# Kernel optimization log

Measured on AMD Instinct MI355X. Metric: run time of the kernel, lower is better.

## Reference

```python
import jax, jax.numpy as jnp
import numpy as np

TOPK = 8
NGRAM = 3
D = 256
VOCAB = 5000


def build_scores_mask(seq_len, topk, ngram):
    # Replicates PREFIX.__init__ mask construction then the [:S*k,:S*k] slice
    # and the ~(...) inversion: True = disallowed (masked out).
    # Chunk-level: query chunk i may attend key chunks j in [i-1, i+ngram-2], j != i.
    L = seq_len
    allowed = np.zeros((L, L), dtype=bool)
    for i in range(L):
        for j in range(max(0, i - 1), min(L, i + ngram - 1)):
            if j != i:
                allowed[i, j] = True
    tok = np.kron(allowed, np.ones((topk, topk), dtype=bool))  # (L*k, L*k)
    return jnp.asarray(~tok)


def setup_inputs() -> dict:
    key = jax.random.key(0)
    k1, k2, k3, k4 = jax.random.split(key, 4)
    bsz, seq_len = 64, 128
    na_pred = jax.random.normal(k1, (bsz, seq_len, VOCAB), dtype=jnp.float32)
    emb_table = jax.random.normal(k2, (VOCAB, D), dtype=jnp.float32) * 0.02
    Wq = jax.random.normal(k3, (D, D), dtype=jnp.float32) / np.sqrt(D)
    Wk = jax.random.normal(k4, (D, D), dtype=jnp.float32) / np.sqrt(D)
    bq = jnp.zeros((D,), dtype=jnp.float32)
    bk = jnp.zeros((D,), dtype=jnp.float32)
    return {"bsz": bsz, "seq_len": seq_len, "na_pred": na_pred,
            "emb_table": emb_table, "Wq": Wq, "bq": bq, "Wk": Wk, "bk": bk}


def reference(bsz, seq_len, na_pred, emb_table, Wq, bq, Wk, bk):
    k, g = TOPK, NGRAM
    # top-k prefix candidates and their renormalized probabilities
    probs = jax.nn.softmax(na_pred, axis=-1)                 # (b, S, V)
    na_prefix_prob, na_prefix = jax.lax.top_k(probs, k)     # (b, S, k)
    na_prefix_prob = jax.nn.softmax(na_prefix_prob, axis=-1)
    # gather prefix embeddings (espnet-style sqrt(d) scale)
    prefix_emb = emb_table[na_prefix] * jnp.asarray(np.sqrt(D), na_pred.dtype)  # (b,S,k,D)
    prefix_emb = prefix_emb.reshape(bsz, seq_len * k, D)
    # ScoreAttention over gathered prefixes with ngram block mask
    q = prefix_emb @ Wq + bq
    kk = prefix_emb @ Wk + bk
    scores = jnp.einsum('bqd,bkd->bqk', q, kk) / jnp.asarray(np.sqrt(D), q.dtype)
    mask = build_scores_mask(seq_len, k, g)                  # (S*k, S*k) True=masked
    scores = jnp.where(mask[None], jnp.asarray(-1e9, scores.dtype), scores)
    attn = jax.nn.softmax(scores, axis=-1)                   # (b, S*k, S*k)
    # per-candidate score = incoming attention mass
    na_score = attn.sum(axis=1).reshape(bsz, seq_len, k)
    # elementwise mul with candidate prob, L1 normalize (F.normalize p=1 eps=1e-12)
    prefix_score = na_score * na_prefix_prob
    l1 = jnp.maximum(jnp.sum(jnp.abs(prefix_score), axis=-1, keepdims=True), 1e-12)
    prefix_score = prefix_score / l1                         # (b, S, k)
    # weighted reduce over candidates
    prefix_emb4 = prefix_emb.reshape(bsz, seq_len, k, D)
    scored_prefix = jnp.sum(prefix_emb4 * prefix_score[..., None], axis=2)  # (b, S, D)
    return scored_prefix, prefix_score, na_prefix
```

## Files before the change

### kernel.cpp

```cpp
#include <hip/hip_runtime.h>
#include <math.h>

#define TOPK 8
#define D    256
#define VOCAB 5000
#define BSZ  64
#define SEQ  128
#define ROWS (BSZ*SEQ)
#define NF4  (VOCAB/4)

#define OFF_IDX   0
#define OFF_NPP   262144
#define OFF_M     524288
#define OFF_W     787456
#define OFF_P     790528
#define OFF_NPART 5910528
#define OFF_KBV   6434816

#define OUT_SCORED 0
#define OUT_PS     2097152
#define OUT_IDX    2162688

typedef unsigned long long u64;
typedef unsigned int u32;

__device__ __forceinline__ float wave_fmax(float v) {
    #pragma unroll
    for (int st = 1; st < 64; st <<= 1) v = fmaxf(v, __shfl_xor(v, st, 64));
    return v;
}
__device__ __forceinline__ float wave_fsum(float v) {
    #pragma unroll
    for (int st = 1; st < 64; st <<= 1) v += __shfl_xor(v, st, 64);
    return v;
}
__device__ __forceinline__ u64 wave_umax(u64 v) {
    #pragma unroll
    for (int st = 1; st < 64; st <<= 1) {
        const u64 o = __shfl_xor(v, st, 64);
        v = (o > v) ? o : v;
    }
    return v;
}
__device__ __forceinline__ u64 pack_key(float x, int idx) {
    u32 bu = __float_as_uint(x);
    u32 key = bu ^ ((u32)((int)bu >> 31) | 0x80000000u);
    return ((u64)key << 32) | (u64)(0xFFFFFFFFu ^ (u32)idx);
}

__global__ __launch_bounds__(256) void topk_kernel(
    const float* __restrict__ na_pred,
    int*  __restrict__ out_idx,
    float* __restrict__ out_npp,
    float* __restrict__ out_idx_f)
{
    __shared__ float tmax[256];
    __shared__ float wsum[4];
    __shared__ float cv[64];
    __shared__ int   ci[64];
    __shared__ int   cnt;
    __shared__ u64   res_s[8];
    __shared__ u64   ured[4];

    const int tid  = threadIdx.x;
    const int lane = tid & 63;
    const int wid  = tid >> 6;
    const long long base = (long long)blockIdx.x * VOCAB;
    const float4* src = (const float4*)(na_pred + base);

    if (tid == 0) cnt = 0;

    const int i0 = tid, i1 = tid + 256, i2 = tid + 512, i3 = tid + 768, i4 = tid + 1024;
    const float4 r0 = src[i0];
    const float4 r1 = src[i1];
    const float4 r2 = src[i2];
    const float4 r3 = src[i3];
    const float4 r4 = (i4 < NF4) ? src[i4]
                    : make_float4(-INFINITY, -INFINITY, -INFINITY, -INFINITY);

    float m01 = fmaxf(fmaxf(r0.x, r0.y), fmaxf(r0.z, r0.w));
    float m23 = fmaxf(fmaxf(r1.x, r1.y), fmaxf(r1.z, r1.w));
    float m45 = fmaxf(fmaxf(r2.x, r2.y), fmaxf(r2.z, r2.w));
    float m67 = fmaxf(fmaxf(r3.x, r3.y), fmaxf(r3.z, r3.w));
    float m89 = fmaxf(fmaxf(r4.x, r4.y), fmaxf(r4.z, r4.w));
    const float m = fmaxf(fmaxf(fmaxf(m01, m23), fmaxf(m45, m67)), m89);
    tmax[tid] = m;
    __syncthreads();

    const float comb = fmaxf(fmaxf(tmax[lane], tmax[lane + 64]),
                             fmaxf(tmax[lane + 128], tmax[lane + 192]));
    const float rowmax = wave_fmax(comb);
    float am = comb, thr = rowmax;
    #pragma unroll
    for (int r = 0; r < 8; ++r) {
        const float cur = wave_fmax(am);
        if (am == cur) am = -INFINITY;
        thr = cur;
    }

    float se = 0.f;
    se += __expf(r0.x - rowmax); se += __expf(r0.y - rowmax);
    se += __expf(r0.z - rowmax); se += __expf(r0.w - rowmax);
    se += __expf(r1.x - rowmax); se += __expf(r1.y - rowmax);
    se += __expf(r1.z - rowmax); se += __expf(r1.w - rowmax);
    se += __expf(r2.x - rowmax); se += __expf(r2.y - rowmax);
    se += __expf(r2.z - rowmax); se += __expf(r2.w - rowmax);
    se += __expf(r3.x - rowmax); se += __expf(r3.y - rowmax);
    se += __expf(r3.z - rowmax); se += __expf(r3.w - rowmax);
    se += __expf(r4.x - rowmax); se += __expf(r4.y - rowmax);
    se += __expf(r4.z - rowmax); se += __expf(r4.w - rowmax);
    const float swv = wave_fsum(se);
    if (lane == 0) wsum[wid] = swv;

#define FILT(val, eidx) do { const float x_ = (val); \
    if (x_ >= thr) { const int pos = atomicAdd(&cnt, 1); \
        if (pos < 64) { cv[pos] = x_; ci[pos] = (eidx); } } } while (0)
    FILT(r0.x, 4*i0+0); FILT(r0.y, 4*i0+1); FILT(r0.z, 4*i0+2); FILT(r0.w, 4*i0+3);
    FILT(r1.x, 4*i1+0); FILT(r1.y, 4*i1+1); FILT(r1.z, 4*i1+2); FILT(r1.w, 4*i1+3);
    FILT(r2.x, 4*i2+0); FILT(r2.y, 4*i2+1); FILT(r2.z, 4*i2+2); FILT(r2.w, 4*i2+3);
    FILT(r3.x, 4*i3+0); FILT(r3.y, 4*i3+1); FILT(r3.z, 4*i3+2); FILT(r3.w, 4*i3+3);
    FILT(r4.x, 4*i4+0); FILT(r4.y, 4*i4+1); FILT(r4.z, 4*i4+2); FILT(r4.w, 4*i4+3);
#undef FILT
    __syncthreads();

    const int cntv = cnt;
    if (cntv <= 64) {
        if (tid < 64) {
            u64 key = (tid < cntv) ? pack_key(cv[tid], ci[tid]) : 0ULL;
            #pragma unroll
            for (int r = 0; r < 8; ++r) {
                const u64 mm = wave_umax(key);
                if (key == mm) key = 0ULL;
                if (tid == 0) res_s[r] = mm;
            }
        }
    } else {
        u64 last = ~0ULL;
        for (int r = 0; r < 8; ++r) {
            u64 best = 0ULL;
#define CAND(val, eidx) do { const u64 k_ = pack_key((val), (eidx)); \
    if (k_ < last && k_ > best) best = k_; } while (0)
            CAND(r0.x, 4*i0+0); CAND(r0.y, 4*i0+1); CAND(r0.z, 4*i0+2); CAND(r0.w, 4*i0+3);
            CAND(r1.x, 4*i1+0); CAND(r1.y, 4*i1+1); CAND(r1.z, 4*i1+2); CAND(r1.w, 4*i1+3);
            CAND(r2.x, 4*i2+0); CAND(r2.y, 4*i2+1); CAND(r2.z, 4*i2+2); CAND(r2.w, 4*i2+3);
            CAND(r3.x, 4*i3+0); CAND(r3.y, 4*i3+1); CAND(r3.z, 4*i3+2); CAND(r3.w, 4*i3+3);
            CAND(r4.x, 4*i4+0); CAND(r4.y, 4*i4+1); CAND(r4.z, 4*i4+2); CAND(r4.w, 4*i4+3);
#undef CAND
            best = wave_umax(best);
            if (lane == 0) ured[wid] = best;
            __syncthreads();
            u64 b = ured[0];
            #pragma unroll
            for (int wq = 1; wq < 4; ++wq) b = (ured[wq] > b) ? ured[wq] : b;
            if (tid == 0) res_s[r] = b;
            last = b;
            __syncthreads();
        }
    }
    __syncthreads();

    if (wid == 0 && lane < 8) {
        const float S = wsum[0] + wsum[1] + wsum[2] + wsum[3];
        const u64 res = res_s[lane];
        const u32 key = (u32)(res >> 32);
        const int ixv = (int)(0xFFFFFFFFu ^ (u32)(res & 0xFFFFFFFFu));
        const u32 bu  = key ^ ((key & 0x80000000u) ? 0x80000000u : 0xFFFFFFFFu);
        const float p = __expf(__uint_as_float(bu) - rowmax) / S;
        float pm = p;
        #pragma unroll
        for (int st = 1; st < 8; st <<= 1) pm = fmaxf(pm, __shfl_xor(pm, st, 64));
        const float q = __expf(p - pm);
        float s2 = q;
        #pragma unroll
        for (int st = 1; st < 8; st <<= 1) s2 += __shfl_xor(s2, st, 64);
        const long long ob = (long long)blockIdx.x * TOPK + lane;
        out_idx[ob]   = ixv;
        out_npp[ob]   = q / s2;
        out_idx_f[ob] = (float)ixv;
    }
}

__global__ __launch_bounds__(256) void m_kernel(
    const float* __restrict__ Wq, const float* __restrict__ Wk,
    float* __restrict__ M)
{
    __shared__ float qrow[D];
    const int a = blockIdx.x, j = threadIdx.x;
    qrow[j] = Wq[a*D + j];
    __syncthreads();
    float acc = 0.f;
    #pragma unroll 4
    for (int d4 = 0; d4 < 64; ++d4) {
        const float4 wk = *(const float4*)&Wk[j*D + 4*d4];
        const float4 q4 = *(const float4*)&qrow[4*d4];
        acc += wk.x*q4.x + wk.y*q4.y + wk.z*q4.z + wk.w*q4.w;
    }
    M[a*D + j] = acc;
}

__global__ __launch_bounds__(256) void bias_kernel(
    const float* __restrict__ Wk, const float* __restrict__ bq,
    float* __restrict__ w)
{
    const int i = threadIdx.x;
    float aw = 0.f;
    #pragma unroll 4
    for (int d4 = 0; d4 < 64; ++d4) {
        const float4 wk = *(const float4*)&Wk[i*D + 4*d4];
        const float4 b4 = *(const float4*)&bq[4*d4];
        aw += wk.x*b4.x + wk.y*b4.y + wk.z*b4.z + wk.w*b4.w;
    }
    w[i] = aw;
}

__global__ __launch_bounds__(256) void kbv_kernel(
    const float* __restrict__ E, const float* __restrict__ w,
    float* __restrict__ kbv)
{
    const int row  = blockIdx.x * 4 + (threadIdx.x >> 6);
    const int lane = threadIdx.x & 63;
    if (row >= VOCAB) return;
    const float4 e  = *(const float4*)&E[(long long)row*D + 4*lane];
    const float4 ww = *(const float4*)&w[4*lane];
    float p = e.x*ww.x + e.y*ww.y + e.z*ww.z + e.w*ww.w;
    #pragma unroll
    for (int st = 1; st < 64; st <<= 1) p += __shfl_xor(p, st, 64);
    if (lane == 0) kbv[row] = p;
}

__global__ __launch_bounds__(256) void p_kernel(
    const float* __restrict__ E, const float* __restrict__ M,
    float* __restrict__ P)
{
    __shared__ float seT[256][20];
    const int tid = threadIdx.x;
    const int r0  = blockIdx.x * 16;
    {
        const int r = tid >> 4, d4b = tid & 15;
        const bool ok = (r0 + r) < VOCAB;
        #pragma unroll
        for (int k = 0; k < 4; ++k) {
            const int d4 = d4b + 16*k;
            float4 v = make_float4(0.f, 0.f, 0.f, 0.f);
            if (ok) v = *(const float4*)&E[(long long)(r0+r)*D + 4*d4];
            seT[4*d4+0][r] = v.x; seT[4*d4+1][r] = v.y;
            seT[4*d4+2][r] = v.z; seT[4*d4+3][r] = v.w;
        }
    }
    __syncthreads();
    const int rg = tid >> 6, j4 = tid & 63;
    float acc[4][4];
    #pragma unroll
    for (int i = 0; i < 4; ++i)
        { acc[i][0]=0.f; acc[i][1]=0.f; acc[i][2]=0.f; acc[i][3]=0.f; }
    #pragma unroll 4
    for (int d = 0; d < 256; ++d) {
        const float4 m4 = *(const float4*)&M[d*D + 4*j4];
        const float4 s4 = *(const float4*)&seT[d][4*rg];
        const float ss[4] = {s4.x, s4.y, s4.z, s4.w};
        #pragma unroll
        for (int rr = 0; rr < 4; ++rr) {
            acc[rr][0] += ss[rr]*m4.x; acc[rr][1] += ss[rr]*m4.y;
            acc[rr][2] += ss[rr]*m4.z; acc[rr][3] += ss[rr]*m4.w;
        }
    }
    #pragma unroll
    for (int rr = 0; rr < 4; ++rr) {
        const int row = r0 + 4*rg + rr;
        if (row < VOCAB) {
            float4 o;
            o.x = acc[rr][0]; o.y = acc[rr][1]; o.z = acc[rr][2]; o.w = acc[rr][3];
            *(float4*)&P[(long long)row*D + 4*j4] = o;
        }
    }
}

__global__ __launch_bounds__(64) void attn_kernel(
    const float* __restrict__ P, const float* __restrict__ E,
    const int*  __restrict__ idx, const float* __restrict__ kbv,
    float* __restrict__ na_part )
{
    const int blk = blockIdx.x;
    const int b = blk >> 7, s = blk & 127;
    const int tid = threadIdx.x;

    __shared__ float Ps[8][260];
    __shared__ float Es[16][260];
    __shared__ int   qidx[8];
    __shared__ int   kidx[16];
    __shared__ float kb[16];
    __shared__ int   kchs[2];

    int kcl[2]; int nk = 0;
    if (s > 0)       kcl[nk++] = s - 1;
    if (s < SEQ - 1) kcl[nk++] = s + 1;
    const int nkeys = nk * 8;

    if (tid < 2 && tid < nk) kchs[tid] = kcl[tid];
    if (tid < 8) qidx[tid] = idx[blk*8 + tid];
    if (tid < 16) {
        if (tid < nkeys) {
            const int v = idx[(b*SEQ + kcl[tid >> 3])*8 + (tid & 7)];
            kidx[tid] = v;
            kb[tid]   = kbv[v];
        } else { kidx[tid] = 0; kb[tid] = 0.f; }
    }
    __syncthreads();

    #pragma unroll
    for (int r = 0; r < 8; ++r)
        *(float4*)&Ps[r][4*tid] = *(const float4*)&P[(long long)qidx[r]*D + 4*tid];
    for (int r = 0; r < 16; ++r)
        if (r < nkeys)
            *(float4*)&Es[r][4*tid] = *(const float4*)&E[(long long)kidx[r]*D + 4*tid];
    __syncthreads();

    const int qp = tid >> 4, ki = tid & 15;
    float acc0 = 0.f, acc1 = 0.f;
    const float* pr0 = Ps[qp];
    const float* pr1 = Ps[qp + 4];
    const float* er  = Es[ki];
    #pragma unroll 4
    for (int d4 = 0; d4 < 64; ++d4) {
        const float4 e  = *(const float4*)&er[4*d4];
        const float4 p0 = *(const float4*)&pr0[4*d4];
        const float4 p1 = *(const float4*)&pr1[4*d4];
        acc0 += p0.x*e.x + p0.y*e.y + p0.z*e.z + p0.w*e.w;
        acc1 += p1.x*e.x + p1.y*e.y + p1.z*e.z + p1.w*e.w;
    }
    const bool kvalid = ki < nkeys;
    const float s0 = kvalid ? (16.f*acc0 + kb[ki]) : -1e30f;
    const float s1 = kvalid ? (16.f*acc1 + kb[ki]) : -1e30f;

    float m0 = s0, m1 = s1;
    #pragma unroll
    for (int st = 1; st < 16; st <<= 1) {
        m0 = fmaxf(m0, __shfl_xor(m0, st, 64));
        m1 = fmaxf(m1, __shfl_xor(m1, st, 64));
    }
    float e0 = kvalid ? __expf(s0 - m0) : 0.f;
    float e1 = kvalid ? __expf(s1 - m1) : 0.f;
    float t0 = e0, t1 = e1;
    #pragma unroll
    for (int st = 1; st < 16; st <<= 1) {
        t0 += __shfl_xor(t0, st, 64);
        t1 += __shfl_xor(t1, st, 64);
    }
    const float a0 = e0 / t0, a1 = e1 / t1;

    float cs = a0 + a1;
    cs += __shfl_xor(cs, 16, 64);
    cs += __shfl_xor(cs, 32, 64);
    if (tid < 16 && kvalid) {
        const int kc   = kchs[tid >> 3];
        const int slot = (kc == s + 1) ? 0 : 1;
        na_part[((b*SEQ + kc)*2 + slot)*8 + (tid & 7)] = cs;
    }
}

__global__ __launch_bounds__(256) void finalize_kernel(
    const float* __restrict__ E, const int* __restrict__ idx,
    const float* __restrict__ npp, const float* __restrict__ na_part,
    float* __restrict__ out)
{
    const int blk = blockIdx.x;
    const int tid = threadIdx.x;
    __shared__ float ps[8];
    __shared__ int   id8[8];

    if (tid < 8) {
        const long long t = (long long)blk*8 + tid;
        const float ns = na_part[((long long)blk*2 + 0)*8 + tid]
                       + na_part[((long long)blk*2 + 1)*8 + tid];
        ps[tid] = ns * npp[t];
        id8[tid] = idx[t];
    }
    __syncthreads();
    if (tid == 0) {
        float l1 = 0.f;
        #pragma unroll
        for (int r = 0; r < 8; ++r) l1 += fabsf(ps[r]);
        l1 = fmaxf(l1, 1e-12f);
        #pragma unroll
        for (int r = 0; r < 8; ++r) ps[r] /= l1;
    }
    __syncthreads();

    float acc = 0.f;
    #pragma unroll
    for (int r = 0; r < 8; ++r) acc += E[(long long)id8[r]*D + tid] * ps[r];
    out[OUT_SCORED + (long long)blk*D + tid] = acc * 16.f;
    if (tid < 8) out[OUT_PS + (long long)blk*8 + tid] = ps[tid];
}

extern "C" void kernel_launch(void* const* d_in, const int* in_sizes, int n_in,
                              void* d_out, int out_size, void* d_ws, size_t ws_size,
                              hipStream_t stream)
{
    const float* na_pred = (const float*)d_in[2];
    const float* emb     = (const float*)d_in[3];
    const float* Wq      = (const float*)d_in[4];
    const float* bq      = (const float*)d_in[5];
    const float* Wk      = (const float*)d_in[6];
    const float* bk      = (const float*)d_in[7];
    (void)bk;

    char* ws = (char*)d_ws;
    int*   ws_idx = (int*)  (ws + OFF_IDX);
    float* ws_npp = (float*)(ws + OFF_NPP);
    float* ws_M   = (float*)(ws + OFF_M);
    float* ws_w   = (float*)(ws + OFF_W);
    float* ws_P   = (float*)(ws + OFF_P);
    float* ws_np  = (float*)(ws + OFF_NPART);
    float* ws_kbv = (float*)(ws + OFF_KBV);
    float* out    = (float*)d_out;

    topk_kernel<<<ROWS, 256, 0, stream>>>(na_pred, ws_idx, ws_npp, out + OUT_IDX);
    m_kernel<<<D, 256, 0, stream>>>(Wq, Wk, ws_M);
    bias_kernel<<<1, 256, 0, stream>>>(Wk, bq, ws_w);
    kbv_kernel<<<(VOCAB + 3)/4, 256, 0, stream>>>(emb, ws_w, ws_kbv);
    p_kernel<<<(VOCAB + 15)/16, 256, 0, stream>>>(emb, ws_M, ws_P);
    hipMemsetAsync(ws_np, 0, BSZ*SEQ*2*8*sizeof(float), stream);
    attn_kernel<<<ROWS, 64, 0, stream>>>(ws_P, emb, ws_idx, ws_kbv, ws_np);
    finalize_kernel<<<ROWS, 256, 0, stream>>>(emb, ws_idx, ws_npp, ws_np, out);
}
```

Before: 134.0 us.

## Rework top-k selection with rank counting and prefix scan, merge small kernels

In the top-k kernel, the 8-round wave-max threshold search is replaced by a shared-memory rank count. The atomic-based candidate filter becomes a wave prefix scan that gives deterministic slots, and the final selection ranks candidates instead of doing repeated wave reductions. The M and bias kernels are merged into one launch. The memset of the attention partials is removed, and finalize now reads only the slots that are actually written at the sequence edges. This is meant to cut serial shuffle chains, atomics and launch overhead, at the cost of more barriers and an O(64) loop per lane.

```diff
diff --git a/kernel.cpp b/kernel.cpp
--- a/kernel.cpp
+++ b/kernel.cpp
@@ -24,11 +24,6 @@
 typedef unsigned long long u64;
 typedef unsigned int u32;
 
-__device__ __forceinline__ float wave_fmax(float v) {
-    #pragma unroll
-    for (int st = 1; st < 64; st <<= 1) v = fmaxf(v, __shfl_xor(v, st, 64));
-    return v;
-}
 __device__ __forceinline__ float wave_fsum(float v) {
     #pragma unroll
     for (int st = 1; st < 64; st <<= 1) v += __shfl_xor(v, st, 64);
@@ -55,10 +50,11 @@
     float* __restrict__ out_idx_f)
 {
     __shared__ float tmax[256];
+    __shared__ float comb_s[64];
     __shared__ float wsum[4];
-    __shared__ float cv[64];
-    __shared__ int   ci[64];
-    __shared__ int   cnt;
+    __shared__ int   wtot[4];
+    __shared__ u64   ck[64];
+    __shared__ float s_rowmax, s_thr;
     __shared__ u64   res_s[8];
     __shared__ u64   ured[4];
 
@@ -68,7 +64,7 @@
     const long long base = (long long)blockIdx.x * VOCAB;
     const float4* src = (const float4*)(na_pred + base);
 
-    if (tid == 0) cnt = 0;
+    if (tid < 8) res_s[tid] = 0xFFFFFFFFULL;
 
     const int i0 = tid, i1 = tid + 256, i2 = tid + 512, i3 = tid + 768, i4 = tid + 1024;
     const float4 r0 = src[i0];
@@ -78,64 +74,91 @@
     const float4 r4 = (i4 < NF4) ? src[i4]
                     : make_float4(-INFINITY, -INFINITY, -INFINITY, -INFINITY);
 
-    float m01 = fmaxf(fmaxf(r0.x, r0.y), fmaxf(r0.z, r0.w));
-    float m23 = fmaxf(fmaxf(r1.x, r1.y), fmaxf(r1.z, r1.w));
-    float m45 = fmaxf(fmaxf(r2.x, r2.y), fmaxf(r2.z, r2.w));
-    float m67 = fmaxf(fmaxf(r3.x, r3.y), fmaxf(r3.z, r3.w));
-    float m89 = fmaxf(fmaxf(r4.x, r4.y), fmaxf(r4.z, r4.w));
+    const float m01 = fmaxf(fmaxf(r0.x, r0.y), fmaxf(r0.z, r0.w));
+    const float m23 = fmaxf(fmaxf(r1.x, r1.y), fmaxf(r1.z, r1.w));
+    const float m45 = fmaxf(fmaxf(r2.x, r2.y), fmaxf(r2.z, r2.w));
+    const float m67 = fmaxf(fmaxf(r3.x, r3.y), fmaxf(r3.z, r3.w));
+    const float m89 = fmaxf(fmaxf(r4.x, r4.y), fmaxf(r4.z, r4.w));
     const float m = fmaxf(fmaxf(fmaxf(m01, m23), fmaxf(m45, m67)), m89);
     tmax[tid] = m;
     __syncthreads();
 
-    const float comb = fmaxf(fmaxf(tmax[lane], tmax[lane + 64]),
-                             fmaxf(tmax[lane + 128], tmax[lane + 192]));
-    const float rowmax = wave_fmax(comb);
-    float am = comb, thr = rowmax;
-    #pragma unroll
-    for (int r = 0; r < 8; ++r) {
-        const float cur = wave_fmax(am);
-        if (am == cur) am = -INFINITY;
-        thr = cur;
-    }
+    if (tid < 64)
+        comb_s[tid] = fmaxf(fmaxf(tmax[tid], tmax[tid + 64]),
+                            fmaxf(tmax[tid + 128], tmax[tid + 192]));
+    __syncthreads();
+
+    if (tid < 64) {
+        const float mine = comb_s[tid];
+        int c = 0;
+        #pragma unroll 8
+        for (int j = 0; j < 64; ++j) {
+            const float o = comb_s[j];
+            c += (o > mine || (o == mine && j < tid)) ? 1 : 0;
+        }
+        if (c == 0) s_rowmax = mine;
+        if (c == 7) s_thr    = mine;
+    }
+    __syncthreads();
+
+    const float rowmax = s_rowmax, thr = s_thr;
 
     float se = 0.f;
-    se += __expf(r0.x - rowmax); se += __expf(r0.y - rowmax);
-    se += __expf(r0.z - rowmax); se += __expf(r0.w - rowmax);
-    se += __expf(r1.x - rowmax); se += __expf(r1.y - rowmax);
-    se += __expf(r1.z - rowmax); se += __expf(r1.w - rowmax);
-    se += __expf(r2.x - rowmax); se += __expf(r2.y - rowmax);
-    se += __expf(r2.z - rowmax); se += __expf(r2.w - rowmax);
-    se += __expf(r3.x - rowmax); se += __expf(r3.y - rowmax);
-    se += __expf(r3.z - rowmax); se += __expf(r3.w - rowmax);
-    se += __expf(r4.x - rowmax); se += __expf(r4.y - rowmax);
-    se += __expf(r4.z - rowmax); se += __expf(r4.w - rowmax);
+    se += __expf(r0.x - rowmax) + __expf(r0.y - rowmax)
+        + __expf(r0.z - rowmax) + __expf(r0.w - rowmax);
+    se += __expf(r1.x - rowmax) + __expf(r1.y - rowmax)
+        + __expf(r1.z - rowmax) + __expf(r1.w - rowmax);
+    se += __expf(r2.x - rowmax) + __expf(r2.y - rowmax)
+        + __expf(r2.z - rowmax) + __expf(r2.w - rowmax);
+    se += __expf(r3.x - rowmax) + __expf(r3.y - rowmax)
+        + __expf(r3.z - rowmax) + __expf(r3.w - rowmax);
+    se += __expf(r4.x - rowmax) + __expf(r4.y - rowmax)
+        + __expf(r4.z - rowmax) + __expf(r4.w - rowmax);
     const float swv = wave_fsum(se);
     if (lane == 0) wsum[wid] = swv;
 
-#define FILT(val, eidx) do { const float x_ = (val); \
-    if (x_ >= thr) { const int pos = atomicAdd(&cnt, 1); \
-        if (pos < 64) { cv[pos] = x_; ci[pos] = (eidx); } } } while (0)
-    FILT(r0.x, 4*i0+0); FILT(r0.y, 4*i0+1); FILT(r0.z, 4*i0+2); FILT(r0.w, 4*i0+3);
-    FILT(r1.x, 4*i1+0); FILT(r1.y, 4*i1+1); FILT(r1.z, 4*i1+2); FILT(r1.w, 4*i1+3);
-    FILT(r2.x, 4*i2+0); FILT(r2.y, 4*i2+1); FILT(r2.z, 4*i2+2); FILT(r2.w, 4*i2+3);
-    FILT(r3.x, 4*i3+0); FILT(r3.y, 4*i3+1); FILT(r3.z, 4*i3+2); FILT(r3.w, 4*i3+3);
-    FILT(r4.x, 4*i4+0); FILT(r4.y, 4*i4+1); FILT(r4.z, 4*i4+2); FILT(r4.w, 4*i4+3);
-#undef FILT
-    __syncthreads();
-
-    const int cntv = cnt;
+    int ct = 0;
+    ct += (r0.x >= thr) + (r0.y >= thr) + (r0.z >= thr) + (r0.w >= thr);
+    ct += (r1.x >= thr) + (r1.y >= thr) + (r1.z >= thr) + (r1.w >= thr);
+    ct += (r2.x >= thr) + (r2.y >= thr) + (r2.z >= thr) + (r2.w >= thr);
+    ct += (r3.x >= thr) + (r3.y >= thr) + (r3.z >= thr) + (r3.w >= thr);
+    ct += (r4.x >= thr) + (r4.y >= thr) + (r4.z >= thr) + (r4.w >= thr);
+
+    int v = ct;
+    #pragma unroll
+    for (int d = 1; d < 64; d <<= 1) {
+        const int o = __shfl_up(v, d, 64);
+        if (lane >= d) v += o;
+    }
+    if (lane == 63) wtot[wid] = v;
+    __syncthreads();
+
+    const int cntv = wtot[0] + wtot[1] + wtot[2] + wtot[3];
+    if (cntv <= 64) {
+        int run = v - ct;
+        #pragma unroll
+        for (int wq = 0; wq < 4; ++wq) if (wq < wid) run += wtot[wq];
+#define STORE(val, eidx) do { const float x_ = (val); \
+        if (x_ >= thr) { ck[run] = pack_key(x_, (eidx)); ++run; } } while (0)
+        STORE(r0.x, 4*i0+0); STORE(r0.y, 4*i0+1); STORE(r0.z, 4*i0+2); STORE(r0.w, 4*i0+3);
+        STORE(r1.x, 4*i1+0); STORE(r1.y, 4*i1+1); STORE(r1.z, 4*i1+2); STORE(r1.w, 4*i1+3);
+        STORE(r2.x, 4*i2+0); STORE(r2.y, 4*i2+1); STORE(r2.z, 4*i2+2); STORE(r2.w, 4*i2+3);
+        STORE(r3.x, 4*i3+0); STORE(r3.y, 4*i3+1); STORE(r3.z, 4*i3+2); STORE(r3.w, 4*i3+3);
+        STORE(r4.x, 4*i4+0); STORE(r4.y, 4*i4+1); STORE(r4.z, 4*i4+2); STORE(r4.w, 4*i4+3);
+#undef STORE
+    }
+    __syncthreads();
+
     if (cntv <= 64) {
         if (tid < 64) {
-            u64 key = (tid < cntv) ? pack_key(cv[tid], ci[tid]) : 0ULL;
-            #pragma unroll
-            for (int r = 0; r < 8; ++r) {
-                const u64 mm = wave_umax(key);
-                if (key == mm) key = 0ULL;
-                if (tid == 0) res_s[r] = mm;
-            }
+            const u64 mine = (tid < cntv) ? ck[tid] : 0ULL;
+            int c = 0;
+            for (int j = 0; j < cntv; ++j) c += (ck[j] > mine) ? 1 : 0;
+            if (tid < cntv && c < 8) res_s[c] = mine;
         }
     } else {
         u64 last = ~0ULL;
+        #pragma unroll 1
         for (int r = 0; r < 8; ++r) {
             u64 best = 0ULL;
 #define CAND(val, eidx) do { const u64 k_ = pack_key((val), (eidx)); \
@@ -180,37 +203,35 @@
     }
 }
 
-__global__ __launch_bounds__(256) void m_kernel(
+__global__ __launch_bounds__(256) void mw_kernel(
     const float* __restrict__ Wq, const float* __restrict__ Wk,
-    float* __restrict__ M)
+    const float* __restrict__ bq,
+    float* __restrict__ M, float* __restrict__ w)
 {
     __shared__ float qrow[D];
-    const int a = blockIdx.x, j = threadIdx.x;
-    qrow[j] = Wq[a*D + j];
-    __syncthreads();
-    float acc = 0.f;
-    #pragma unroll 4
-    for (int d4 = 0; d4 < 64; ++d4) {
-        const float4 wk = *(const float4*)&Wk[j*D + 4*d4];
-        const float4 q4 = *(const float4*)&qrow[4*d4];
-        acc += wk.x*q4.x + wk.y*q4.y + wk.z*q4.z + wk.w*q4.w;
-    }
-    M[a*D + j] = acc;
-}
-
-__global__ __launch_bounds__(256) void bias_kernel(
-    const float* __restrict__ Wk, const float* __restrict__ bq,
-    float* __restrict__ w)
-{
-    const int i = threadIdx.x;
-    float aw = 0.f;
-    #pragma unroll 4
-    for (int d4 = 0; d4 < 64; ++d4) {
-        const float4 wk = *(const float4*)&Wk[i*D + 4*d4];
-        const float4 b4 = *(const float4*)&bq[4*d4];
-        aw += wk.x*b4.x + wk.y*b4.y + wk.z*b4.z + wk.w*b4.w;
-    }
-    w[i] = aw;
+    const int j = threadIdx.x;
+    if (blockIdx.x < D) {
+        const int a = blockIdx.x;
+        qrow[j] = Wq[a*D + j];
+        __syncthreads();
+        float acc = 0.f;
+        #pragma unroll 4
+        for (int d4 = 0; d4 < 64; ++d4) {
+            const float4 wk = *(const float4*)&Wk[j*D + 4*d4];
+            const float4 q4 = *(const float4*)&qrow[4*d4];
+            acc += wk.x*q4.x + wk.y*q4.y + wk.z*q4.z + wk.w*q4.w;
+        }
+        M[a*D + j] = acc;
+    } else {
+        float aw = 0.f;
+        #pragma unroll 4
+        for (int d4 = 0; d4 < 64; ++d4) {
+            const float4 wk = *(const float4*)&Wk[j*D + 4*d4];
+            const float4 b4 = *(const float4*)&bq[4*d4];
+            aw += wk.x*b4.x + wk.y*b4.y + wk.z*b4.z + wk.w*b4.w;
+        }
+        w[j] = aw;
+    }
 }
 
 __global__ __launch_bounds__(256) void kbv_kernel(
@@ -364,14 +385,16 @@
     float* __restrict__ out)
 {
     const int blk = blockIdx.x;
+    const int s   = blk & 127;
     const int tid = threadIdx.x;
     __shared__ float ps[8];
     __shared__ int   id8[8];
 
     if (tid < 8) {
         const long long t = (long long)blk*8 + tid;
-        const float ns = na_part[((long long)blk*2 + 0)*8 + tid]
-                       + na_part[((long long)blk*2 + 1)*8 + tid];
+        float ns = 0.f;
+        if (s >= 1)       ns += na_part[((long long)blk*2 + 0)*8 + tid];
+        if (s <= SEQ - 2) ns += na_part[((long long)blk*2 + 1)*8 + tid];
         ps[tid] = ns * npp[t];
         id8[tid] = idx[t];
     }
@@ -416,11 +439,9 @@
     float* out    = (float*)d_out;
 
     topk_kernel<<<ROWS, 256, 0, stream>>>(na_pred, ws_idx, ws_npp, out + OUT_IDX);
-    m_kernel<<<D, 256, 0, stream>>>(Wq, Wk, ws_M);
-    bias_kernel<<<1, 256, 0, stream>>>(Wk, bq, ws_w);
+    mw_kernel<<<D + 1, 256, 0, stream>>>(Wq, Wk, bq, ws_M, ws_w);
     kbv_kernel<<<(VOCAB + 3)/4, 256, 0, stream>>>(emb, ws_w, ws_kbv);
     p_kernel<<<(VOCAB + 15)/16, 256, 0, stream>>>(emb, ws_M, ws_P);
-    hipMemsetAsync(ws_np, 0, BSZ*SEQ*2*8*sizeof(float), stream);
     attn_kernel<<<ROWS, 64, 0, stream>>>(ws_P, emb, ws_idx, ws_kbv, ws_np);
     finalize_kernel<<<ROWS, 256, 0, stream>>>(emb, ws_idx, ws_npp, ws_np, out);
 }
```

New measurement: 126.2 us. 1.06x faster.
